# Kernel tuning notes

Hardware: AMD Instinct MI355X
Metric: run time of the kernel (lower is better)

The kernel has to match this reference:

```python
import jax, jax.numpy as jnp
import numpy as np

A = 128       # atom_fea_len
NBR = 41      # nbr_fea_len
H = 128       # h_fea_len_dist == h_fea_len_const
NCONV = 3
EPS = 1e-5    # BatchNorm eps


def leaky(x):
    return jnp.where(x >= 0, x, 0.01 * x)  # LeakyReLU(0.01)


def bn(x2d, g, b):
    # training-mode BatchNorm1d: batch statistics over dim 0 (biased variance)
    mu = x2d.mean(0)
    var = x2d.var(0)
    return g * (x2d - mu) * jax.lax.rsqrt(var + EPS) + b


def setup_inputs() -> dict:
    N, M = 20000, 12
    key = jax.random.key(0)
    ks = jax.random.split(key, 24)
    s = 0.02
    in2 = 2 * A + NBR  # 297
    d = {}
    d["atom_fea"] = jax.random.normal(ks[0], (N, 92), jnp.float32)
    d["nbr_fea"] = jax.random.uniform(ks[1], (N, M, NBR), dtype=jnp.float32)
    d["nbr_fea_offset"] = jax.random.normal(ks[2], (N, M, 3), jnp.float32)
    d["atom_pos"] = jax.random.normal(ks[3], (N, 3), jnp.float32) * 3.0
    d["cells"] = jnp.eye(3, dtype=jnp.float32) * 10.0 + 0.1 * jax.random.normal(ks[4], (3, 3), jnp.float32)
    d["nbr_fea_idx"] = jax.random.randint(ks[5], (N, M), 0, N)
    # embedding
    d["emb_W"] = s * jax.random.normal(ks[6], (A, 92), jnp.float32)
    d["emb_b"] = jnp.zeros((A,), jnp.float32)
    # conv layers (stacked)
    d["convs_W"] = s * jax.random.normal(ks[7], (NCONV, 2 * A, in2), jnp.float32)
    d["convs_b"] = jnp.zeros((NCONV, 2 * A), jnp.float32)
    d["convs_bn1_g"] = jnp.ones((NCONV, 2 * A), jnp.float32)
    d["convs_bn1_b"] = jnp.zeros((NCONV, 2 * A), jnp.float32)
    d["convs_bn2_g"] = jnp.ones((NCONV, A), jnp.float32)
    d["convs_bn2_b"] = jnp.zeros((NCONV, A), jnp.float32)
    # bond_distance head
    d["dist_W"] = s * jax.random.normal(ks[8], (H, in2), jnp.float32)
    d["dist_b"] = jnp.zeros((H,), jnp.float32)
    d["dist_bn_g"] = jnp.ones((H,), jnp.float32)
    d["dist_bn_b"] = jnp.zeros((H,), jnp.float32)
    d["dist2_W"] = s * jax.random.normal(ks[9], (1, H), jnp.float32)
    d["dist2_b"] = jnp.zeros((1,), jnp.float32)
    # bond_constant head
    d["const_W"] = s * jax.random.normal(ks[10], (H, in2), jnp.float32)
    d["const_b"] = jnp.zeros((H,), jnp.float32)
    d["const_bn_g"] = jnp.ones((H,), jnp.float32)
    d["const_bn_b"] = jnp.zeros((H,), jnp.float32)
    d["const2_W"] = s * jax.random.normal(ks[11], (1, H), jnp.float32)
    d["const2_b"] = jnp.zeros((1,), jnp.float32)
    return d


def _forward(atom_fea, nbr_fea, nbr_fea_offset, atom_pos, cells,
             emb_W, emb_b, convs_W, convs_b, convs_bn1_g, convs_bn1_b,
             convs_bn2_g, convs_bn2_b, dist_W, dist_b, dist_bn_g, dist_bn_b,
             dist2_W, dist2_b, const_W, const_b, const_bn_g, const_bn_b,
             const2_W, const2_b, nbr_fea_idx):
    N, M = nbr_fea_idx.shape
    af = atom_fea @ emb_W.T + emb_b  # (N, A) embedding

    # get_distance: PBC distance using fractional offsets and the cell matrix
    nbr_abs = atom_pos[nbr_fea_idx] + jnp.einsum('nmk,kd->nmd', nbr_fea_offset, cells)
    dvec = nbr_abs - atom_pos[:, None, :]
    distance = jnp.sqrt(jnp.sum(dvec * dvec, -1, keepdims=True) + 1e-12)  # (N, M, 1)

    # conv layers: gather -> concat -> linear -> bn -> gate -> sum -> bn -> residual
    for i in range(NCONV):
        total = jnp.concatenate([
            jnp.broadcast_to(af[:, None, :], (N, M, A)),
            af[nbr_fea_idx],
            nbr_fea], axis=2)                                   # (N, M, 2A+NBR)
        g = jnp.einsum('nmf,of->nmo', total, convs_W[i]) + convs_b[i]  # (N, M, 2A)
        g = bn(g.reshape(-1, 2 * A), convs_bn1_g[i], convs_bn1_b[i]).reshape(N, M, 2 * A)
        nbr_filter = jax.nn.sigmoid(g[..., :A])
        nbr_core = leaky(g[..., A:])
        summed = bn((nbr_filter * nbr_core).sum(1), convs_bn2_g[i], convs_bn2_b[i])
        af = leaky(af + summed)

    # bond features
    bond_fea = jnp.concatenate([
        jnp.broadcast_to(af[:, None, :], (N, M, A)),
        af[nbr_fea_idx],
        nbr_fea], axis=2)  # (N, M, 2A+NBR)

    # bond_distance head (LeakyReLU activations)
    bd = jnp.einsum('nmf,hf->nmh', bond_fea, dist_W) + dist_b
    bd = leaky(bn(bd.reshape(-1, H), dist_bn_g, dist_bn_b).reshape(N, M, H))
    bd = leaky(jnp.einsum('nmh,oh->nmo', bd, dist2_W) + dist2_b + distance)  # (N, M, 1)

    # bond_constant head (Softplus activations)
    bc = jnp.einsum('nmf,hf->nmh', bond_fea, const_W) + const_b
    bc = jax.nn.softplus(bn(bc.reshape(-1, H), const_bn_g, const_bn_b).reshape(N, M, H))
    bc = jax.nn.softplus(jnp.einsum('nmh,oh->nmo', bc, const2_W) + const2_b)  # (N, M, 1)

    return jnp.concatenate([bd, bc], axis=-1)  # (N, M, 2)


def reference(atom_fea, nbr_fea, nbr_fea_offset, atom_pos, cells,
              emb_W, emb_b, convs_W, convs_b, convs_bn1_g, convs_bn1_b,
              convs_bn2_g, convs_bn2_b, dist_W, dist_b, dist_bn_g, dist_bn_b,
              dist2_W, dist2_b, const_W, const_b, const_bn_g, const_bn_b,
              const2_W, const2_b, nbr_fea_idx):
    return _forward(atom_fea, nbr_fea, nbr_fea_offset, atom_pos, cells,
                    emb_W, emb_b, convs_W, convs_b, convs_bn1_g, convs_bn1_b,
                    convs_bn2_g, convs_bn2_b, dist_W, dist_b, dist_bn_g, dist_bn_b,
                    dist2_W, dist2_b, const_W, const_b, const_bn_g, const_bn_b,
                    const2_W, const2_b, nbr_fea_idx)
```

## Files before the change

### kernel.cpp

```cpp
#include <hip/hip_runtime.h>
#include <hip/hip_bf16.h>
#include <math.h>

typedef __hip_bfloat16 bf16;

#define AFEA 128
#define NBRF 41
#define IN2 297
#define KP 320
#define ASTR 264
#define TCOL 68
#define P1 64
#define P2 16

typedef __attribute__((ext_vector_type(8))) short bf16x8;
typedef __attribute__((ext_vector_type(4))) float f32x4;

__device__ __forceinline__ unsigned short bfbits(float x) {
    bf16 h = __float2bfloat16(x);
    return *(unsigned short*)&h;
}
__device__ __forceinline__ float us2f(unsigned short u) {
    return __uint_as_float((unsigned int)u << 16);
}
__device__ __forceinline__ unsigned int pack2(float x, float y) {
    return (unsigned int)bfbits(x) | ((unsigned int)bfbits(y) << 16);
}
__device__ __forceinline__ float blo(unsigned int u) { return __uint_as_float(u << 16); }
__device__ __forceinline__ float bhi(unsigned int u) { return __uint_as_float(u & 0xffff0000u); }
__device__ __forceinline__ float leakyf(float x) { return x >= 0.f ? x : 0.01f * x; }
__device__ __forceinline__ float sigmoid_fast(float x) { return 1.f / (1.f + __expf(-x)); }
__device__ __forceinline__ float softplus_fast(float x) {
    return fmaxf(x, 0.f) + __logf(1.f + __expf(-fabsf(x)));
}

__global__ void nbr16_kernel(const float* __restrict__ nbr, unsigned short* __restrict__ nbr16,
                             int NM)
{
    int i = blockIdx.x * blockDim.x + threadIdx.x;
    if (i >= NM * 64) return;
    int k = i & 63, e = i >> 6;
    nbr16[i] = (k < NBRF) ? bfbits(nbr[(size_t)e * NBRF + k]) : 0;
}

__global__ __launch_bounds__(256) void embed_kernel(
    const float* __restrict__ xf, const float* __restrict__ W,
    const float* __restrict__ b, unsigned short* __restrict__ af16, int N)
{
    __shared__ float W_s[92 * 128];
    __shared__ float xs[16 * 92];
    int t = threadIdx.x;
    int n0 = blockIdx.x * 16;
    for (int i = t; i < 92 * 128; i += 256) {
        int o = i / 92, k = i - o * 92;
        W_s[k * 128 + o] = W[i];
    }
    for (int i = t; i < 16 * 92; i += 256) {
        int a = i / 92, k = i - a * 92;
        int n = n0 + a;
        xs[i] = (n < N) ? xf[(size_t)n * 92 + k] : 0.f;
    }
    __syncthreads();
    int o = t & 127, h = t >> 7;
    float bias = b[o];
    for (int a = h; a < 16; a += 2) {
        int n = n0 + a;
        if (n >= N) break;
        float acc = bias;
        const float* xr = xs + a * 92;
        #pragma unroll 4
        for (int k = 0; k < 92; k++) acc += xr[k] * W_s[k * 128 + o];
        af16[(size_t)n * AFEA + o] = bfbits(acc);
    }
}

__global__ void prep_kernel(const float* __restrict__ Wa, size_t offA,
                            const float* __restrict__ Wb2, size_t offB,
                            unsigned short* __restrict__ Wb,
                            float* __restrict__ zbuf, int nz)
{
    int i = blockIdx.x * blockDim.x + threadIdx.x;
    if (i < nz) zbuf[i] = 0.f;
    if (i >= KP * 256) return;
    int t32 = i & 31;
    int c = (i >> 5) & 255;
    int kc = i >> 13;
    int k = kc * 32 + t32;
    float v = 0.f;
    if (k < IN2) v = (c < 128) ? Wa[offA + (size_t)c * IN2 + k]
                               : Wb2[offB + (size_t)(c - 128) * IN2 + k];
    Wb[i] = bfbits(v);
}

__global__ __launch_bounds__(256, 4) void gemm_mfma_kernel(
    const unsigned short* __restrict__ af16, const unsigned short* __restrict__ nbr16,
    const int* __restrict__ idx, const unsigned short* __restrict__ Wb,
    const float* __restrict__ bias_a, size_t boffA,
    const float* __restrict__ bias_b, size_t boffB,
    unsigned short* __restrict__ g_t, float* __restrict__ part1,
    int NM, int M)
{
    __shared__ unsigned short smem[256 * TCOL];
    unsigned short* a_tile = smem;
    const int t = threadIdx.x;
    const int e0 = blockIdx.x * 64;
    const int l = t & 63, w = t >> 6;
    const int m16 = l & 15, q = l >> 4;
    const int colbase = w * 64;
    const unsigned short* bbase = Wb + (size_t)(colbase + m16) * 32 + q * 8;

    {
        int row = t >> 2, p = t & 3;
        int e = e0 + row;
        int n = e / M;
        int j = idx[e];
        const uint4* srcn = (const uint4*)(af16 + (size_t)n * AFEA);
        const uint4* srcj = (const uint4*)(af16 + (size_t)j * AFEA);
        uint4* dst = (uint4*)(a_tile + row * ASTR);
        #pragma unroll
        for (int u = 0; u < 4; u++) dst[p + 4 * u] = srcn[p + 4 * u];
        #pragma unroll
        for (int u = 0; u < 4; u++) dst[16 + p + 4 * u] = srcj[p + 4 * u];
    }

    bf16x8 bcur[4];
    #pragma unroll
    for (int ct = 0; ct < 4; ct++)
        bcur[ct] = *(const bf16x8*)(bbase + ct * 512);

    __syncthreads();

    f32x4 acc[4][4];
    #pragma unroll
    for (int rt = 0; rt < 4; rt++)
        #pragma unroll
        for (int ct = 0; ct < 4; ct++) acc[rt][ct] = (f32x4)0.f;

    const unsigned short* abase = a_tile + m16 * ASTR + q * 8;

    #pragma unroll
    for (int kc = 0; kc < KP / 32; kc++) {
        bf16x8 a[4], bn[4];
        if (kc < KP / 32 - 1) {
            #pragma unroll
            for (int ct = 0; ct < 4; ct++)
                bn[ct] = *(const bf16x8*)(bbase + (kc + 1) * 8192 + ct * 512);
        }
        if (kc < 8) {
            #pragma unroll
            for (int rt = 0; rt < 4; rt++)
                a[rt] = *(const bf16x8*)(abase + rt * 16 * ASTR + kc * 32);
        } else {
            #pragma unroll
            for (int rt = 0; rt < 4; rt++)
                a[rt] = *(const bf16x8*)(nbr16 + (size_t)(e0 + rt * 16 + m16) * 64
                                         + (kc - 8) * 32 + q * 8);
        }
        #pragma unroll
        for (int rt = 0; rt < 4; rt++)
            #pragma unroll
            for (int ct = 0; ct < 4; ct++)
                acc[rt][ct] = __builtin_amdgcn_mfma_f32_16x16x32_bf16(
                    a[rt], bcur[ct], acc[rt][ct], 0, 0, 0);
        if (kc < KP / 32 - 1) {
            #pragma unroll
            for (int ct = 0; ct < 4; ct++) bcur[ct] = bn[ct];
        }
    }

    __syncthreads();

    float* pp = part1 + (size_t)(blockIdx.x & (P1 - 1)) * 512;
    #pragma unroll
    for (int ct = 0; ct < 4; ct++) {
        int col = colbase + ct * 16 + m16;
        float bias = (col < 128) ? bias_a[boffA + col] : bias_b[boffB + col - 128];
        float ps = 0.f, pq = 0.f;
        #pragma unroll
        for (int rt = 0; rt < 4; rt++) {
            float v0 = acc[rt][ct][0] + bias;
            float v1 = acc[rt][ct][1] + bias;
            float v2 = acc[rt][ct][2] + bias;
            float v3 = acc[rt][ct][3] + bias;
            ps += (v0 + v1) + (v2 + v3);
            pq += (v0 * v0 + v1 * v1) + (v2 * v2 + v3 * v3);
            uint2 pk;
            pk.x = pack2(v0, v1);
            pk.y = pack2(v2, v3);
            *(uint2*)(smem + col * TCOL + rt * 16 + q * 4) = pk;
        }
        ps += __shfl_xor(ps, 16); ps += __shfl_xor(ps, 32);
        pq += __shfl_xor(pq, 16); pq += __shfl_xor(pq, 32);
        if (q == 0) {
            atomicAdd(&pp[col], ps);
            atomicAdd(&pp[256 + col], pq);
        }
    }
    __syncthreads();

    #pragma unroll
    for (int r = 0; r < 16; r++) {
        int i = r * 256 + t;
        int col = i >> 4, ch = i & 15;
        uint2 v = *(const uint2*)(smem + col * TCOL + ch * 4);
        *(uint2*)(g_t + (size_t)col * NM + e0 + ch * 4) = v;
    }
}

__global__ __launch_bounds__(256) void gate_kernel(
    const unsigned short* __restrict__ gt, const float* __restrict__ part1,
    const float* __restrict__ gamma, const float* __restrict__ beta,
    float* __restrict__ summed, float* __restrict__ part2,
    float cnt1, int N, int M, int NM)
{
    __shared__ float affA[4 * 16], affC[4 * 16];
    int t = threadIdx.x, w = t >> 6, l = t & 63;
    int cp0 = (blockIdx.x & 3) * 16 + w * 4;
    int fch0 = 2 * cp0;

    if (l < 16) {
        int ch = (l < 8) ? (fch0 + l) : (128 + fch0 + (l - 8));
        float s = 0.f, qq = 0.f;
        #pragma unroll 8
        for (int p = 0; p < P1; p++) {
            s += part1[(size_t)p * 512 + ch];
            qq += part1[(size_t)p * 512 + 256 + ch];
        }
        float mean = s / cnt1;
        float var = fmaxf(qq / cnt1 - mean * mean, 0.f);
        float a = gamma[ch] * rsqrtf(var + 1e-5f);
        affA[w * 16 + l] = a;
        affC[w * 16 + l] = beta[ch] - mean * a;
    }
    __syncthreads();

    int n = (blockIdx.x >> 2) * 64 + l;
    bool act = (n < N);
    size_t col0 = (size_t)n * M;
    float* pp = part2 + (size_t)(blockIdx.x & (P2 - 1)) * 256;
    #pragma unroll
    for (int cpi = 0; cpi < 4; cpi++) {
        int chf = fch0 + 2 * cpi;
        int chc = 128 + chf;
        float s0 = 0.f, s1 = 0.f;
        if (act) {
            const uint2* rf0 = (const uint2*)(gt + (size_t)chf * NM + col0);
            const uint2* rf1 = (const uint2*)(gt + (size_t)(chf + 1) * NM + col0);
            const uint2* rc0 = (const uint2*)(gt + (size_t)chc * NM + col0);
            const uint2* rc1 = (const uint2*)(gt + (size_t)(chc + 1) * NM + col0);
            float aF0 = affA[w * 16 + 2 * cpi],     cF0 = affC[w * 16 + 2 * cpi];
            float aF1 = affA[w * 16 + 2 * cpi + 1], cF1 = affC[w * 16 + 2 * cpi + 1];
            float aC0 = affA[w * 16 + 8 + 2 * cpi],     cC0 = affC[w * 16 + 8 + 2 * cpi];
            float aC1 = affA[w * 16 + 8 + 2 * cpi + 1], cC1 = affC[w * 16 + 8 + 2 * cpi + 1];
            #pragma unroll
            for (int u = 0; u < 3; u++) {
                uint2 f0 = rf0[u], f1 = rf1[u], k0 = rc0[u], k1 = rc1[u];
                #pragma unroll
                for (int h = 0; h < 4; h++) {
                    unsigned int fw0 = (h < 2) ? f0.x : f0.y;
                    unsigned int fw1 = (h < 2) ? f1.x : f1.y;
                    unsigned int kw0 = (h < 2) ? k0.x : k0.y;
                    unsigned int kw1 = (h < 2) ? k1.x : k1.y;
                    float gf0 = (h & 1) ? bhi(fw0) : blo(fw0);
                    float gf1 = (h & 1) ? bhi(fw1) : blo(fw1);
                    float gc0 = (h & 1) ? bhi(kw0) : blo(kw0);
                    float gc1 = (h & 1) ? bhi(kw1) : blo(kw1);
                    s0 += sigmoid_fast(fmaf(aF0, gf0, cF0)) * leakyf(fmaf(aC0, gc0, cC0));
                    s1 += sigmoid_fast(fmaf(aF1, gf1, cF1)) * leakyf(fmaf(aC1, gc1, cC1));
                }
            }
            *(float2*)(summed + (size_t)n * AFEA + chf) = make_float2(s0, s1);
        }
        float q0 = s0 * s0, q1 = s1 * s1;
        #pragma unroll
        for (int sft = 32; sft > 0; sft >>= 1) {
            s0 += __shfl_xor(s0, sft);
            s1 += __shfl_xor(s1, sft);
            q0 += __shfl_xor(q0, sft);
            q1 += __shfl_xor(q1, sft);
        }
        if (l == 0) {
            atomicAdd(&pp[chf], s0);
            atomicAdd(&pp[chf + 1], s1);
            atomicAdd(&pp[128 + chf], q0);
            atomicAdd(&pp[128 + chf + 1], q1);
        }
    }
}

__global__ __launch_bounds__(256) void afup_kernel(
    unsigned short* __restrict__ af16, const float* __restrict__ summed,
    const float* __restrict__ part2,
    const float* __restrict__ gamma2, const float* __restrict__ beta2,
    float cnt2, int total)
{
    __shared__ float a2s[128], c2s[128];
    int t = threadIdx.x;
    if (t < 128) {
        float s = 0.f, qq = 0.f;
        #pragma unroll
        for (int p = 0; p < P2; p++) {
            s += part2[(size_t)p * 256 + t];
            qq += part2[(size_t)p * 256 + 128 + t];
        }
        float mean = s / cnt2;
        float var = fmaxf(qq / cnt2 - mean * mean, 0.f);
        float a = gamma2[t] * rsqrtf(var + 1e-5f);
        a2s[t] = a;
        c2s[t] = beta2[t] - mean * a;
    }
    __syncthreads();
    int o = t & 127;
    float a2 = a2s[o], c2 = c2s[o];
    int base = blockIdx.x * 2048 + t;
    #pragma unroll
    for (int k = 0; k < 8; k++) {
        int i = base + k * 256;
        if (i < total) {
            float v = us2f(af16[i]) + a2 * summed[i] + c2;
            v = (v >= 0.f) ? v : 0.01f * v;
            af16[i] = bfbits(v);
        }
    }
}

__global__ __launch_bounds__(256) void head_kernel(
    const unsigned short* __restrict__ gt, const float* __restrict__ part1,
    const float* __restrict__ dbg, const float* __restrict__ cbg,
    const float* __restrict__ dbb, const float* __restrict__ cbb,
    const float* __restrict__ w2d, const float* __restrict__ b2d,
    const float* __restrict__ w2c, const float* __restrict__ b2c,
    const float* __restrict__ pos, const float* __restrict__ off,
    const float* __restrict__ cells, const int* __restrict__ idx,
    float* __restrict__ out, float cnt1, int NM, int M)
{
    __shared__ float a_s[256], c_s[256], w_s[256];
    int t = threadIdx.x;
    {
        float s = 0.f, qq = 0.f;
        #pragma unroll 8
        for (int p = 0; p < P1; p++) {
            s += part1[(size_t)p * 512 + t];
            qq += part1[(size_t)p * 512 + 256 + t];
        }
        float mean = s / cnt1;
        float var = fmaxf(qq / cnt1 - mean * mean, 0.f);
        float g  = (t < 128) ? dbg[t] : cbg[t - 128];
        float be = (t < 128) ? dbb[t] : cbb[t - 128];
        float a = g * rsqrtf(var + 1e-5f);
        a_s[t] = a;
        c_s[t] = be - mean * a;
        w_s[t] = (t < 128) ? w2d[t] : w2c[t - 128];
    }
    __syncthreads();

    int e = blockIdx.x * 512 + t * 2;
    if (e >= NM) return;
    float sd0 = 0.f, sd1 = 0.f, sc0 = 0.f, sc1 = 0.f;
    #pragma unroll 4
    for (int ch = 0; ch < 128; ch++) {
        unsigned int u = *(const unsigned int*)(gt + (size_t)ch * NM + e);
        float a = a_s[ch], c = c_s[ch], wv = w_s[ch];
        sd0 += leakyf(fmaf(a, blo(u), c)) * wv;
        sd1 += leakyf(fmaf(a, bhi(u), c)) * wv;
    }
    #pragma unroll 4
    for (int ch = 128; ch < 256; ch++) {
        unsigned int u = *(const unsigned int*)(gt + (size_t)ch * NM + e);
        float a = a_s[ch], c = c_s[ch], wv = w_s[ch];
        sc0 += softplus_fast(fmaf(a, blo(u), c)) * wv;
        sc1 += softplus_fast(fmaf(a, bhi(u), c)) * wv;
    }
    float dist[2];
    #pragma unroll
    for (int h = 0; h < 2; h++) {
        int eb = e + h;
        int n = eb / M;
        int j = idx[eb];
        float o0 = off[(size_t)eb * 3 + 0];
        float o1 = off[(size_t)eb * 3 + 1];
        float o2 = off[(size_t)eb * 3 + 2];
        float d0 = o0 * cells[0] + o1 * cells[3] + o2 * cells[6] + pos[(size_t)j * 3 + 0] - pos[(size_t)n * 3 + 0];
        float d1 = o0 * cells[1] + o1 * cells[4] + o2 * cells[7] + pos[(size_t)j * 3 + 1] - pos[(size_t)n * 3 + 1];
        float d2 = o0 * cells[2] + o1 * cells[5] + o2 * cells[8] + pos[(size_t)j * 3 + 2] - pos[(size_t)n * 3 + 2];
        dist[h] = sqrtf(d0 * d0 + d1 * d1 + d2 * d2 + 1e-12f);
    }
    float bd = b2d[0], bc = b2c[0];
    float4 o4;
    o4.x = leakyf(sd0 + bd + dist[0]);
    o4.y = softplus_fast(sc0 + bc);
    o4.z = leakyf(sd1 + bd + dist[1]);
    o4.w = softplus_fast(sc1 + bc);
    *(float4*)(out + (size_t)e * 2) = o4;
}

extern "C" void kernel_launch(void* const* d_in, const int* in_sizes, int n_in,
                              void* d_out, int out_size, void* d_ws, size_t ws_size,
                              hipStream_t stream) {
    const float* atom_fea   = (const float*)d_in[0];
    const float* nbr_fea    = (const float*)d_in[1];
    const float* nbr_off    = (const float*)d_in[2];
    const float* atom_pos   = (const float*)d_in[3];
    const float* cells      = (const float*)d_in[4];
    const int*   idx        = (const int*)d_in[5];
    const float* emb_W      = (const float*)d_in[6];
    const float* emb_b      = (const float*)d_in[7];
    const float* convs_W    = (const float*)d_in[8];
    const float* convs_b    = (const float*)d_in[9];
    const float* bn1g       = (const float*)d_in[10];
    const float* bn1b       = (const float*)d_in[11];
    const float* bn2g       = (const float*)d_in[12];
    const float* bn2b       = (const float*)d_in[13];
    const float* dist_W     = (const float*)d_in[14];
    const float* dist_b     = (const float*)d_in[15];
    const float* dist_bn_g  = (const float*)d_in[16];
    const float* dist_bn_b  = (const float*)d_in[17];
    const float* dist2_W    = (const float*)d_in[18];
    const float* dist2_b    = (const float*)d_in[19];
    const float* const_W    = (const float*)d_in[20];
    const float* const_b    = (const float*)d_in[21];
    const float* const_bn_g = (const float*)d_in[22];
    const float* const_bn_b = (const float*)d_in[23];
    const float* const2_W   = (const float*)d_in[24];
    const float* const2_b   = (const float*)d_in[25];

    const int N  = in_sizes[0] / 92;
    const int M  = in_sizes[5] / N;
    const int NM = N * M;

    char* ws = (char*)d_ws;
    size_t off = 0;
    unsigned short* af16  = (unsigned short*)(ws + off); off += (size_t)N * AFEA * 2;
    float* summed         = (float*)(ws + off); off += (size_t)N * AFEA * 4;
    unsigned short* Wb    = (unsigned short*)(ws + off); off += (size_t)256 * KP * 2;
    float* part1          = (float*)(ws + off); off += (size_t)P1 * 512 * 4;
    float* part2          = (float*)(ws + off); off += (size_t)P2 * 256 * 4;
    unsigned short* g_t   = (unsigned short*)(ws + off); off += (size_t)NM * 256 * 2;
    unsigned short* nbr16 = (unsigned short*)(ws + off); off += (size_t)NM * 64 * 2;

    const int NPART = P1 * 512 + P2 * 256;

    nbr16_kernel<<<(NM * 64 + 255) / 256, 256, 0, stream>>>(nbr_fea, nbr16, NM);
    embed_kernel<<<(N + 15) / 16, 256, 0, stream>>>(atom_fea, emb_W, emb_b, af16, N);

    const int gblocks = NM / 64;
    const int gateblocks = ((N + 63) / 64) * 4;
    const int prepblocks = (256 * KP + 255) / 256;

    for (int i = 0; i < 3; i++) {
        size_t wo  = (size_t)i * 256 * IN2;
        size_t bo  = (size_t)i * 256;
        size_t b2o = (size_t)i * 128;

        prep_kernel<<<prepblocks, 256, 0, stream>>>(
            convs_W, wo, convs_W, wo + (size_t)128 * IN2, Wb, part1, NPART);
        gemm_mfma_kernel<<<gblocks, 256, 0, stream>>>(
            af16, nbr16, idx, Wb, convs_b, bo, convs_b, bo + 128,
            g_t, part1, NM, M);
        gate_kernel<<<gateblocks, 256, 0, stream>>>(
            g_t, part1, bn1g + bo, bn1b + bo, summed, part2, (float)NM, N, M, NM);
        afup_kernel<<<(N * AFEA + 2047) / 2048, 256, 0, stream>>>(
            af16, summed, part2, bn2g + b2o, bn2b + b2o, (float)N, N * AFEA);
    }

    {
        prep_kernel<<<prepblocks, 256, 0, stream>>>(
            dist_W, 0, const_W, 0, Wb, part1, P1 * 512);
        gemm_mfma_kernel<<<gblocks, 256, 0, stream>>>(
            af16, nbr16, idx, Wb, dist_b, 0, const_b, 0,
            g_t, part1, NM, M);
        head_kernel<<<(NM + 511) / 512, 256, 0, stream>>>(
            g_t, part1, dist_bn_g, const_bn_g, dist_bn_b, const_bn_b,
            dist2_W, dist2_b, const2_W, const2_b,
            atom_pos, nbr_off, cells, idx, (float*)d_out, (float)NM, NM, M);
    }
}
```

Before: 693.4 us.

## Convert all layer weights in one prep launch and remap GEMM tiles per XCD

Replaces the four per-layer prep kernels with a single launch that converts all conv and head weights to bf16 and zeros all partial-sum buffers up front, using separate per-layer partial buffers. It also remaps GEMM block indices so consecutive tiles land on the same group of blocks (blockIdx & 7 chunking), which is meant to improve L2 locality across the MI355X's XCDs for the gathered atom rows. This removes three kernel launches and their serialization from the timed stream, in exchange for a slightly larger workspace and a padded grid with a few early-exit blocks.

```diff
diff --git a/kernel.cpp b/kernel.cpp
--- a/kernel.cpp
+++ b/kernel.cpp
@@ -74,22 +74,28 @@
     }
 }
 
-__global__ void prep_kernel(const float* __restrict__ Wa, size_t offA,
-                            const float* __restrict__ Wb2, size_t offB,
-                            unsigned short* __restrict__ Wb,
-                            float* __restrict__ zbuf, int nz)
+__global__ void prepall_kernel(const float* __restrict__ convs_W,
+                               const float* __restrict__ dist_W,
+                               const float* __restrict__ const_W,
+                               unsigned short* __restrict__ Wb_all,
+                               float* __restrict__ zbuf, int nz)
 {
     int i = blockIdx.x * blockDim.x + threadIdx.x;
     if (i < nz) zbuf[i] = 0.f;
-    if (i >= KP * 256) return;
-    int t32 = i & 31;
-    int c = (i >> 5) & 255;
-    int kc = i >> 13;
+    if (i >= 4 * KP * 256) return;
+    int s = i / (KP * 256);
+    int ii = i - s * (KP * 256);
+    int t32 = ii & 31;
+    int c = (ii >> 5) & 255;
+    int kc = ii >> 13;
     int k = kc * 32 + t32;
     float v = 0.f;
-    if (k < IN2) v = (c < 128) ? Wa[offA + (size_t)c * IN2 + k]
-                               : Wb2[offB + (size_t)(c - 128) * IN2 + k];
-    Wb[i] = bfbits(v);
+    if (k < IN2) {
+        if (s < 3) v = convs_W[(size_t)s * 256 * IN2 + (size_t)c * IN2 + k];
+        else       v = (c < 128) ? dist_W[(size_t)c * IN2 + k]
+                                 : const_W[(size_t)(c - 128) * IN2 + k];
+    }
+    Wb_all[i] = bfbits(v);
 }
 
 __global__ __launch_bounds__(256, 4) void gemm_mfma_kernel(
@@ -100,10 +106,15 @@
     unsigned short* __restrict__ g_t, float* __restrict__ part1,
     int NM, int M)
 {
+    const int ntiles = NM / 64;
+    const int per = (ntiles + 7) >> 3;
+    const int tile = (blockIdx.x & 7) * per + (blockIdx.x >> 3);
+    if (tile >= ntiles) return;
+
     __shared__ unsigned short smem[256 * TCOL];
     unsigned short* a_tile = smem;
     const int t = threadIdx.x;
-    const int e0 = blockIdx.x * 64;
+    const int e0 = tile * 64;
     const int l = t & 63, w = t >> 6;
     const int m16 = l & 15, q = l >> 4;
     const int colbase = w * 64;
@@ -170,7 +181,7 @@
 
     __syncthreads();
 
-    float* pp = part1 + (size_t)(blockIdx.x & (P1 - 1)) * 512;
+    float* pp = part1 + (size_t)(tile & (P1 - 1)) * 512;
     #pragma unroll
     for (int ct = 0; ct < 4; ct++) {
         int col = colbase + ct * 16 + m16;
@@ -430,47 +441,47 @@
 
     char* ws = (char*)d_ws;
     size_t off = 0;
-    unsigned short* af16  = (unsigned short*)(ws + off); off += (size_t)N * AFEA * 2;
-    float* summed         = (float*)(ws + off); off += (size_t)N * AFEA * 4;
-    unsigned short* Wb    = (unsigned short*)(ws + off); off += (size_t)256 * KP * 2;
-    float* part1          = (float*)(ws + off); off += (size_t)P1 * 512 * 4;
-    float* part2          = (float*)(ws + off); off += (size_t)P2 * 256 * 4;
-    unsigned short* g_t   = (unsigned short*)(ws + off); off += (size_t)NM * 256 * 2;
-    unsigned short* nbr16 = (unsigned short*)(ws + off); off += (size_t)NM * 64 * 2;
-
-    const int NPART = P1 * 512 + P2 * 256;
+    unsigned short* af16   = (unsigned short*)(ws + off); off += (size_t)N * AFEA * 2;
+    float* summed          = (float*)(ws + off); off += (size_t)N * AFEA * 4;
+    unsigned short* Wb_all = (unsigned short*)(ws + off); off += (size_t)4 * KP * 256 * 2;
+    float* part1_all       = (float*)(ws + off); off += (size_t)4 * P1 * 512 * 4;
+    float* part2_all       = (float*)(ws + off); off += (size_t)3 * P2 * 256 * 4;
+    unsigned short* g_t    = (unsigned short*)(ws + off); off += (size_t)NM * 256 * 2;
+    unsigned short* nbr16  = (unsigned short*)(ws + off); off += (size_t)NM * 64 * 2;
+
+    const int NZALL = 4 * P1 * 512 + 3 * P2 * 256;
 
     nbr16_kernel<<<(NM * 64 + 255) / 256, 256, 0, stream>>>(nbr_fea, nbr16, NM);
     embed_kernel<<<(N + 15) / 16, 256, 0, stream>>>(atom_fea, emb_W, emb_b, af16, N);
-
-    const int gblocks = NM / 64;
+    prepall_kernel<<<(4 * KP * 256 + 255) / 256, 256, 0, stream>>>(
+        convs_W, dist_W, const_W, Wb_all, part1_all, NZALL);
+
+    const int ntiles = NM / 64;
+    const int gpad = ((ntiles + 7) / 8) * 8;
     const int gateblocks = ((N + 63) / 64) * 4;
-    const int prepblocks = (256 * KP + 255) / 256;
 
     for (int i = 0; i < 3; i++) {
-        size_t wo  = (size_t)i * 256 * IN2;
         size_t bo  = (size_t)i * 256;
         size_t b2o = (size_t)i * 128;
-
-        prep_kernel<<<prepblocks, 256, 0, stream>>>(
-            convs_W, wo, convs_W, wo + (size_t)128 * IN2, Wb, part1, NPART);
-        gemm_mfma_kernel<<<gblocks, 256, 0, stream>>>(
-            af16, nbr16, idx, Wb, convs_b, bo, convs_b, bo + 128,
-            g_t, part1, NM, M);
+        float* p1 = part1_all + (size_t)i * P1 * 512;
+        float* p2 = part2_all + (size_t)i * P2 * 256;
+
+        gemm_mfma_kernel<<<gpad, 256, 0, stream>>>(
+            af16, nbr16, idx, Wb_all + (size_t)i * KP * 256,
+            convs_b, bo, convs_b, bo + 128, g_t, p1, NM, M);
         gate_kernel<<<gateblocks, 256, 0, stream>>>(
-            g_t, part1, bn1g + bo, bn1b + bo, summed, part2, (float)NM, N, M, NM);
+            g_t, p1, bn1g + bo, bn1b + bo, summed, p2, (float)NM, N, M, NM);
         afup_kernel<<<(N * AFEA + 2047) / 2048, 256, 0, stream>>>(
-            af16, summed, part2, bn2g + b2o, bn2b + b2o, (float)N, N * AFEA);
+            af16, summed, p2, bn2g + b2o, bn2b + b2o, (float)N, N * AFEA);
     }
 
     {
-        prep_kernel<<<prepblocks, 256, 0, stream>>>(
-            dist_W, 0, const_W, 0, Wb, part1, P1 * 512);
-        gemm_mfma_kernel<<<gblocks, 256, 0, stream>>>(
-            af16, nbr16, idx, Wb, dist_b, 0, const_b, 0,
-            g_t, part1, NM, M);
+        float* p1 = part1_all + (size_t)3 * P1 * 512;
+        gemm_mfma_kernel<<<gpad, 256, 0, stream>>>(
+            af16, nbr16, idx, Wb_all + (size_t)3 * KP * 256,
+            dist_b, 0, const_b, 0, g_t, p1, NM, M);
         head_kernel<<<(NM + 511) / 512, 256, 0, stream>>>(
-            g_t, part1, dist_bn_g, const_bn_g, dist_bn_b, const_bn_b,
+            g_t, p1, dist_bn_g, const_bn_g, dist_bn_b, const_bn_b,
             dist2_W, dist2_b, const2_W, const2_b,
             atom_pos, nbr_off, cells, idx, (float*)d_out, (float)NM, NM, M);
     }
```

Result: slower. 726.5 us (+4.8%).
